# Kernel optimization log

Measured on AMD Instinct MI355X. Metric: run time of the kernel, lower is better.

## Reference

```python
import jax, jax.numpy as jnp
import numpy as np

EPS_NORM = 1e-12  # F.normalize eps
EPS_LOG = 1e-10
COMMITMENT_COST = 0.25


def setup_inputs() -> dict:
    key = jax.random.key(0)
    k1, k2 = jax.random.split(key)
    x = jax.random.normal(k1, (32, 256, 32, 32), dtype=jnp.float32)
    # nn.Embedding weight init: uniform(-1, 1)
    W = jax.random.uniform(k2, (1024, 256), dtype=jnp.float32, minval=-1.0, maxval=1.0)
    return {"x": x, "W": W, "n": 2}


def reference(x, W, n):
    sg = jax.lax.stop_gradient
    # NCHW -> NHWC
    inputs = jnp.transpose(x, (0, 2, 3, 1))
    B, H, Wd, D = inputs.shape
    K = W.shape[0]
    flat = inputs.reshape(-1, D)                       # [N, D]
    N = flat.shape[0]
    # squared euclidean distances via matmul: [N, K]
    distances = (jnp.sum(flat * flat, axis=1, keepdims=True)
                 + jnp.sum(W * W, axis=1)
                 - 2.0 * jnp.matmul(flat, W.T))
    # topk of -distances -> n smallest distances
    neg_vals, encoding_indices = jax.lax.top_k(-distances, n)  # [N, n]
    inv_dist = 1.0 / (-neg_vals)                        # 1/distance, [N, n]
    norm = jnp.maximum(jnp.sqrt(jnp.sum(inv_dist * inv_dist, axis=-1, keepdims=True)), EPS_NORM)
    weights = sg(inv_dist / norm)                       # detached in torch
    # scatter weights into one-hot-ish encodings [N, K]
    rows = jnp.arange(N)[:, None]
    encodings = jnp.zeros((N, K), dtype=flat.dtype).at[rows, encoding_indices].set(weights)
    quantized = jnp.matmul(encodings, W).reshape(B, H, Wd, D)
    e_latent_loss = jnp.mean((sg(quantized) - inputs) ** 2)
    q_latent_loss = jnp.mean((quantized - sg(inputs)) ** 2)
    loss = q_latent_loss + COMMITMENT_COST * e_latent_loss
    # straight-through
    quantized_st = inputs + sg(quantized - inputs)
    avg_probs = jnp.mean(encodings, axis=0)
    perplexity = jnp.exp(-jnp.sum(avg_probs * jnp.log(avg_probs + EPS_LOG)))
    return loss, jnp.transpose(quantized_st, (0, 3, 1, 2)), perplexity, encodings
```

## Files before the change

kernel.cpp:

```cpp
#include <hip/hip_runtime.h>
#include <math.h>

#define NROWS 32768
#define DIMS  256
#define KCODES 1024

typedef __attribute__((ext_vector_type(8))) short short8;
typedef __attribute__((ext_vector_type(4))) float f32x4;

static const size_t OFF_WB     = 8388608;
static const size_t OFF_WNORM  = OFF_WB + 131072;
static const size_t OFF_ENCSUM = OFF_WNORM + 1024;
static const size_t OFF_LOSSP  = OFF_ENCSUM + 1024;
static const size_t OFF_WND    = OFF_LOSSP + 8192;

static const size_t OUT_Q    = 1;
static const size_t OUT_PERP = 8388609;
static const size_t OUT_ENC  = 8388610;

__device__ inline unsigned short f2bf(float f) {
    unsigned int u = __float_as_uint(f);
    unsigned int r = u + 0x7FFFu + ((u >> 16) & 1u);
    return (unsigned short)(r >> 16);
}

__device__ inline float packdi(float d, int code) {
    return __uint_as_float((__float_as_uint(d) & 0xFFFFFC00u) | (unsigned)code);
}

__device__ __forceinline__ void gl_lds16(const void* gsrc, void* ldst) {
    typedef const __attribute__((address_space(1))) unsigned int GU;
    typedef __attribute__((address_space(3))) unsigned int LU;
    __builtin_amdgcn_global_load_lds((GU*)gsrc, (LU*)ldst, 16, 0, 0);
}

__global__ __launch_bounds__(256) void wprep(const float* __restrict__ Wm,
                                             unsigned short* __restrict__ Wb,
                                             float* __restrict__ wnorm,
                                             double* __restrict__ wnormd,
                                             float* __restrict__ enc_sum)
{
    const int r = blockIdx.x * 4 + (threadIdx.x >> 6);
    const int lane = threadIdx.x & 63;
    float4 v = ((const float4*)(Wm + (size_t)r * 256))[lane];
    ushort4 o;
    o.x = f2bf(v.x); o.y = f2bf(v.y); o.z = f2bf(v.z); o.w = f2bf(v.w);
    const int d0 = lane * 4;
    const int kk = d0 >> 5, quad = (d0 >> 3) & 3, jb = d0 & 7;
    const int tt = r >> 4, col = r & 15;
    const size_t idx = (size_t)tt * 4096 + (size_t)((kk * 4 + quad) * 16 + col) * 8 + jb;
    *(ushort4*)(Wb + idx) = o;
    double s = (double)v.x*(double)v.x + (double)v.y*(double)v.y
             + (double)v.z*(double)v.z + (double)v.w*(double)v.w;
    #pragma unroll
    for (int off = 32; off > 0; off >>= 1) s += __shfl_down(s, off);
    if (lane == 0) { wnormd[r] = s; wnorm[r] = (float)s; }
    if (blockIdx.x == 0) {
        #pragma unroll
        for (int q = 0; q < 4; ++q) enc_sum[threadIdx.x * 4 + q] = 0.0f;
    }
}

__global__ __launch_bounds__(256, 4) void gemm_topk_quant(
    const float* __restrict__ x, const unsigned short* __restrict__ Wb,
    const float* __restrict__ wnorm, const double* __restrict__ wnd,
    const float* __restrict__ Wm,
    float* __restrict__ enc_sum,
    float* __restrict__ enc,
    float* __restrict__ outq, float* __restrict__ loss_part)
{
    __shared__ __align__(16) char lds[36864];
    float*  sCd   = (float*)lds;
    int*    mIdx  = (int*)(lds + 13312);
    double* rd    = (double*)(lds + 14336);
    float*  qtile = (float*)lds;
    double* rnr   = (double*)(lds + 33792);
    int*    s0    = (int*)(lds + 34048);
    int*    s1    = (int*)(lds + 34176);
    float*  sw0   = (float*)(lds + 34304);
    float*  sw1   = (float*)(lds + 34432);
    double* sredd = (double*)(lds + 34560);
    unsigned short* xtile = (unsigned short*)(lds + 16384);
    float*  wnLds = (float*)(lds + 32768);

    const int t    = threadIdx.x;
    const int wave = t >> 6;
    const int g    = wave & 1;
    const int h    = wave >> 1;
    const int lane = t & 63;
    const int col  = lane & 15;
    const int quad = lane >> 4;
    const int r0   = blockIdx.x * 32;
    const int b    = r0 >> 10;
    const int hw0  = r0 & 1023;
    const float* xblk = x + (size_t)b * 262144 + hw0;

    const int row = t >> 3;
    const int q8  = t & 7;

    const char* wb_bytes = (const char*)Wb;
    {
        const char* src = wb_bytes + (size_t)(h * 32) * 8192 + g * 4096;
        char* dstl = lds + h * 8192 + g * 4096;
        #pragma unroll
        for (int q = 0; q < 4; ++q)
            gl_lds16(src + q * 1024 + lane * 16, dstl + q * 1024);
        gl_lds16((const char*)wnorm + wave * 1024 + lane * 16,
                 (char*)wnLds + wave * 1024);
    }

    float xs[32];
    {
        const float* xr = xblk + row;
        #pragma unroll
        for (int c = 0; c < 8; ++c)
            #pragma unroll
            for (int k = 0; k < 4; ++k)
                xs[c * 4 + k] = xr[(size_t)(c * 32 + q8 * 4 + k) * 1024];
    }

    #pragma unroll
    for (int c = 0; c < 8; ++c) {
        ushort4 o;
        o.x = f2bf(xs[c * 4 + 0]);
        o.y = f2bf(xs[c * 4 + 1]);
        o.z = f2bf(xs[c * 4 + 2]);
        o.w = f2bf(xs[c * 4 + 3]);
        const int xi = (row * 256 + c * 32 + q8 * 4) ^ ((row & 7) << 3);
        *(ushort4*)(xtile + xi) = o;
    }
    __syncthreads();

    short8 af[8];
    #pragma unroll
    for (int kk = 0; kk < 8; ++kk) {
        const int xi = ((g * 16 + col) * 256 + kk * 32 + quad * 8) ^ ((col & 7) << 3);
        af[kk] = *(const short8*)(xtile + xi);
    }
    __syncthreads();

    float m0[4], m1[4], m2[4];
    #pragma unroll
    for (int r = 0; r < 4; ++r) { m0[r] = 3.4e38f; m1[r] = 3.4e38f; m2[r] = 3.4e38f; }

    const f32x4 zero4 = {0.f, 0.f, 0.f, 0.f};
    for (int cc = 0; cc < 32; ++cc) {
        if (cc < 31) {
            const char* src = wb_bytes + (size_t)(h * 32 + cc + 1) * 8192 + g * 4096;
            char* dstl = lds + ((cc + 1) & 1) * 16384 + h * 8192 + g * 4096;
            #pragma unroll
            for (int q = 0; q < 4; ++q)
                gl_lds16(src + q * 1024 + lane * 16, dstl + q * 1024);
        }
        *(f32x4*)(enc + (size_t)(r0 + cc) * KCODES + t * 4) = zero4;

        const char* bb = lds + (cc & 1) * 16384 + h * 8192;
        f32x4 acc_a = {0.f, 0.f, 0.f, 0.f};
        f32x4 acc_b = {0.f, 0.f, 0.f, 0.f};
        #pragma unroll
        for (int kk = 0; kk < 4; ++kk) {
            short8 b0 = *(const short8*)(bb + kk * 1024 + lane * 16);
            short8 b1 = *(const short8*)(bb + (kk + 4) * 1024 + lane * 16);
            acc_a = __builtin_amdgcn_mfma_f32_16x16x32_bf16(af[kk], b0, acc_a, 0, 0, 0);
            acc_b = __builtin_amdgcn_mfma_f32_16x16x32_bf16(af[kk + 4], b1, acc_b, 0, 0, 0);
        }
        const int code0 = h * 512 + cc * 16 + col;
        const float wn0 = wnLds[code0];
        #pragma unroll
        for (int r = 0; r < 4; ++r) {
            float pv0 = packdi(fmaf(-2.0f, acc_a[r] + acc_b[r], wn0), code0);
            m2[r] = __builtin_amdgcn_fmed3f(m1[r], m2[r], pv0);
            m1[r] = __builtin_amdgcn_fmed3f(m0[r], m1[r], pv0);
            m0[r] = fminf(m0[r], pv0);
        }
        __syncthreads();
    }

    #pragma unroll
    for (int r = 0; r < 4; ++r) {
        const int rl = g * 16 + quad * 4 + r;
        const int s  = h * 48 + col * 3;
        sCd[(s + 0) * 34 + rl] = m0[r];
        sCd[(s + 1) * 34 + rl] = m1[r];
        sCd[(s + 2) * 34 + rl] = m2[r];
    }
    __syncthreads();

    {
        float a0 = 3.4e38f, a1 = 3.4e38f, a2 = 3.4e38f, a3 = 3.4e38f,
              a4 = 3.4e38f, a5 = 3.4e38f, a6 = 3.4e38f, a7 = 3.4e38f;
        #pragma unroll
        for (int i = 0; i < 12; ++i) {
            float d = sCd[(q8 * 12 + i) * 34 + row];
            if (d < a7) {
                a7 = d; float tf;
                if (a7 < a6) { tf = a7; a7 = a6; a6 = tf; }
                if (a6 < a5) { tf = a6; a6 = a5; a5 = tf; }
                if (a5 < a4) { tf = a5; a5 = a4; a4 = tf; }
                if (a4 < a3) { tf = a4; a4 = a3; a3 = tf; }
                if (a3 < a2) { tf = a3; a3 = a2; a2 = tf; }
                if (a2 < a1) { tf = a2; a2 = a1; a1 = tf; }
                if (a1 < a0) { tf = a1; a1 = a0; a0 = tf; }
            }
        }
        float sel = 3.4e38f;
        #pragma unroll
        for (int q = 0; q < 8; ++q) {
            float m = a0;
            m = fminf(m, __shfl_xor(m, 1));
            m = fminf(m, __shfl_xor(m, 2));
            m = fminf(m, __shfl_xor(m, 4));
            if (q8 == q) sel = m;
            if (a0 == m) { a0 = a1; a1 = a2; a2 = a3; a3 = a4;
                           a4 = a5; a5 = a6; a6 = a7; a7 = 3.4e38f; }
        }
        mIdx[row * 8 + q8] = (int)(__float_as_uint(sel) & 1023u);
    }
    __syncthreads();

    {
        int cd[8];
        #pragma unroll
        for (int c8 = 0; c8 < 8; ++c8) cd[c8] = mIdx[row * 8 + c8];
        double dot[8];
        #pragma unroll
        for (int c8 = 0; c8 < 8; ++c8) dot[c8] = 0.0;
        double rn = 0.0;
        #pragma unroll
        for (int c = 0; c < 8; ++c) {
            const int d0 = c * 32 + q8 * 4;
            const double x0 = (double)xs[c * 4 + 0];
            const double x1 = (double)xs[c * 4 + 1];
            const double x2 = (double)xs[c * 4 + 2];
            const double x3 = (double)xs[c * 4 + 3];
            rn += x0*x0 + x1*x1 + x2*x2 + x3*x3;
            #pragma unroll
            for (int c8 = 0; c8 < 8; ++c8) {
                const float4 wv = *(const float4*)(Wm + (size_t)cd[c8] * 256 + d0);
                dot[c8] += x0 * (double)wv.x + x1 * (double)wv.y
                         + x2 * (double)wv.z + x3 * (double)wv.w;
            }
        }
        #pragma unroll
        for (int m = 1; m < 8; m <<= 1) {
            #pragma unroll
            for (int c8 = 0; c8 < 8; ++c8) dot[c8] += __shfl_xor(dot[c8], m);
            rn += __shfl_xor(rn, m);
        }
        int myc = 0; double mydot = 0.0;
        #pragma unroll
        for (int c8 = 0; c8 < 8; ++c8)
            if (q8 == c8) { myc = cd[c8]; mydot = dot[c8]; }
        rd[row * 8 + q8] = wnd[myc] - 2.0 * mydot;
        if (q8 == 0) rnr[row] = rn;
    }
    __syncthreads();

    if (t < 32) {
        double rn = rnr[t];
        double d0 = 1e300, d1 = 1e300; int b0 = 1 << 30, b1 = 1 << 30;
        #pragma unroll
        for (int q = 0; q < 8; ++q) {
            double d = rd[t * 8 + q];
            int    c = mIdx[t * 8 + q];
            if (d < d0 || (d == d0 && c < b0)) { d1 = d0; b1 = b0; d0 = d; b0 = c; }
            else if (d < d1 || (d == d1 && c < b1)) { d1 = d; b1 = c; }
        }
        double D0 = rn + d0;
        double D1 = rn + d1;
        double inv0 = 1.0 / D0, inv1 = 1.0 / D1;
        double nrm = sqrt(inv0 * inv0 + inv1 * inv1);
        if (nrm < 1e-12) nrm = 1e-12;
        float w0 = (float)(inv0 / nrm);
        float w1 = (float)(inv1 / nrm);
        s0[t] = b0; s1[t] = b1; sw0[t] = w0; sw1[t] = w1;
        atomicAdd(&enc_sum[b0], w0);
        atomicAdd(&enc_sum[b1], w1);
        enc[(size_t)(r0 + t) * KCODES + b0] = w0;
        enc[(size_t)(r0 + t) * KCODES + b1] = w1;
    }
    __syncthreads();

    double ls = 0.0;
    #pragma unroll
    for (int p2 = 0; p2 < 2; ++p2) {
        const int   cA = s0[row], cB = s1[row];
        const float w0 = sw0[row], w1 = sw1[row];
        #pragma unroll
        for (int cq = 0; cq < 4; ++cq) {
            const int c  = p2 * 4 + cq;
            const int dg = c * 32 + q8 * 4;
            const float4 a  = *(const float4*)(Wm + (size_t)cA * 256 + dg);
            const float4 bv = *(const float4*)(Wm + (size_t)cB * 256 + dg);
            f32x4 qv;
            qv.x = w0 * a.x + w1 * bv.x;
            qv.y = w0 * a.y + w1 * bv.y;
            qv.z = w0 * a.z + w1 * bv.z;
            qv.w = w0 * a.w + w1 * bv.w;
            float e0 = qv.x - xs[c * 4 + 0];
            float e1 = qv.y - xs[c * 4 + 1];
            float e2 = qv.z - xs[c * 4 + 2];
            float e3 = qv.w - xs[c * 4 + 3];
            ls += (double)(e0*e0 + e1*e1 + e2*e2 + e3*e3);
            const int dl = cq * 32 + q8 * 4;
            *(f32x4*)(qtile + row * 132 + dl) = qv;
        }
        __syncthreads();
        #pragma unroll
        for (int p = 0; p < 4; ++p) {
            const int task = p * 256 + t;
            const int cl   = task >> 3;
            const int hwq  = task & 7;
            f32x4 v;
            v.x = qtile[(hwq * 4 + 0) * 132 + cl];
            v.y = qtile[(hwq * 4 + 1) * 132 + cl];
            v.z = qtile[(hwq * 4 + 2) * 132 + cl];
            v.w = qtile[(hwq * 4 + 3) * 132 + cl];
            *(f32x4*)(outq + ((size_t)(b * 256 + p2 * 128 + cl)) * 1024 + hw0 + hwq * 4) = v;
        }
        __syncthreads();
    }

    #pragma unroll
    for (int off = 32; off > 0; off >>= 1) ls += __shfl_down(ls, off);
    if (lane == 0) sredd[wave] = ls;
    __syncthreads();
    if (t == 0) {
        double s = 0.0;
        #pragma unroll
        for (int w = 0; w < 4; ++w) s += sredd[w];
        loss_part[blockIdx.x] = (float)s;
    }
}

__global__ __launch_bounds__(256) void finalize_k(const float* __restrict__ enc_sum,
                                                  const float* __restrict__ loss_part,
                                                  float* __restrict__ out)
{
    __shared__ double sh[256];
    const int t = threadIdx.x;
    double ls = 0.0;
    for (int i = t; i < 1024; i += 256) ls += (double)loss_part[i];
    sh[t] = ls; __syncthreads();
    for (int s = 128; s > 0; s >>= 1) { if (t < s) sh[t] += sh[t + s]; __syncthreads(); }
    double loss_sum = sh[0];
    __syncthreads();
    double ps = 0.0;
    for (int k = t; k < KCODES; k += 256) {
        double p = (double)enc_sum[k] / (double)NROWS;
        ps += p * log(p + 1e-10);
    }
    sh[t] = ps; __syncthreads();
    for (int s = 128; s > 0; s >>= 1) { if (t < s) sh[t] += sh[t + s]; __syncthreads(); }
    if (t == 0) {
        out[0]        = (float)(1.25 * loss_sum / 8388608.0);
        out[OUT_PERP] = (float)exp(-sh[0]);
    }
}

extern "C" void kernel_launch(void* const* d_in, const int* in_sizes, int n_in,
                              void* d_out, int out_size, void* d_ws, size_t ws_size,
                              hipStream_t stream)
{
    const float* x  = (const float*)d_in[0];
    const float* Wm = (const float*)d_in[1];
    float* out = (float*)d_out;
    float* ws  = (float*)d_ws;

    unsigned short* Wb      = (unsigned short*)(ws + OFF_WB);
    float*          wnorm   = ws + OFF_WNORM;
    float*          enc_sum = ws + OFF_ENCSUM;
    float*          loss_p  = ws + OFF_LOSSP;
    double*         wnd     = (double*)(ws + OFF_WND);

    wprep<<<KCODES / 4, 256, 0, stream>>>(Wm, Wb, wnorm, wnd, enc_sum);
    gemm_topk_quant<<<NROWS / 32, 256, 0, stream>>>(x, Wb, wnorm, wnd, Wm, enc_sum,
                                                    out + OUT_ENC, out + OUT_Q, loss_p);
    finalize_k<<<1, 256, 0, stream>>>(enc_sum, loss_p, out);
}
```

Before: 241.2 us.

## Coalesce x loads through an LDS transpose and merge quantized writeback passes

Input rows were read as strided scalar loads. They are now read as float4 vectors along the spatial axis and transposed through a swizzled fp32 LDS bounce buffer. Both the fp32 registers kept for the loss and the bf16 MFMA A-fragments are taken from that buffer, in two halves of the feature dimension. The quantized-output transpose also now uses one full 256-channel LDS tile instead of two half passes, which drops a pair of barriers. The cost is extra LDS traffic, added barriers during the load phase, and a larger LDS tile that has to fit the existing layout.

Result: no change. 238.1 us (-1.3%).

```diff
diff --git a/kernel.cpp b/kernel.cpp
--- a/kernel.cpp
+++ b/kernel.cpp
@@ -80,7 +80,7 @@
     float*  sw0   = (float*)(lds + 34304);
     float*  sw1   = (float*)(lds + 34432);
     double* sredd = (double*)(lds + 34560);
-    unsigned short* xtile = (unsigned short*)(lds + 16384);
+    float*  xbounce = (float*)(lds + 16384);
     float*  wnLds = (float*)(lds + 32768);
 
     const int t    = threadIdx.x;
@@ -110,32 +110,56 @@
     }
 
     float xs[32];
-    {
-        const float* xr = xblk + row;
-        #pragma unroll
-        for (int c = 0; c < 8; ++c)
+    short8 af[8];
+    const int hwq   = t & 7;
+    const int dbase = t >> 3;
+    const int arow  = g * 16 + col;
+    #pragma unroll
+    for (int h2 = 0; h2 < 2; ++h2) {
+        float4 xv0, xv1, xv2, xv3;
+        {
+            const float* xp = xblk + hwq * 4;
+            xv0 = *(const float4*)(xp + (size_t)(h2 * 128 +  0 + dbase) * 1024);
+            xv1 = *(const float4*)(xp + (size_t)(h2 * 128 + 32 + dbase) * 1024);
+            xv2 = *(const float4*)(xp + (size_t)(h2 * 128 + 64 + dbase) * 1024);
+            xv3 = *(const float4*)(xp + (size_t)(h2 * 128 + 96 + dbase) * 1024);
+        }
+        if (h2) __syncthreads();
+        #pragma unroll
+        for (int rr = 0; rr < 4; ++rr) {
+            const float4 xv = (rr == 0) ? xv0 : (rr == 1) ? xv1 : (rr == 2) ? xv2 : xv3;
+            const int dloc = rr * 32 + dbase;
             #pragma unroll
-            for (int k = 0; k < 4; ++k)
-                xs[c * 4 + k] = xr[(size_t)(c * 32 + q8 * 4 + k) * 1024];
-    }
-
-    #pragma unroll
-    for (int c = 0; c < 8; ++c) {
-        ushort4 o;
-        o.x = f2bf(xs[c * 4 + 0]);
-        o.y = f2bf(xs[c * 4 + 1]);
-        o.z = f2bf(xs[c * 4 + 2]);
-        o.w = f2bf(xs[c * 4 + 3]);
-        const int xi = (row * 256 + c * 32 + q8 * 4) ^ ((row & 7) << 3);
-        *(ushort4*)(xtile + xi) = o;
-    }
-    __syncthreads();
-
-    short8 af[8];
-    #pragma unroll
-    for (int kk = 0; kk < 8; ++kk) {
-        const int xi = ((g * 16 + col) * 256 + kk * 32 + quad * 8) ^ ((col & 7) << 3);
-        af[kk] = *(const short8*)(xtile + xi);
+            for (int j = 0; j < 4; ++j) {
+                const int hw = hwq * 4 + j;
+                const float vj = (j == 0) ? xv.x : (j == 1) ? xv.y : (j == 2) ? xv.z : xv.w;
+                xbounce[(hw * 128 + dloc) ^ ((hw & 7) << 2)] = vj;
+            }
+        }
+        __syncthreads();
+        #pragma unroll
+        for (int c2 = 0; c2 < 4; ++c2) {
+            const int w = (row * 128 + c2 * 32 + q8 * 4) ^ ((row & 7) << 2);
+            f32x4 v = *(const f32x4*)(xbounce + w);
+            xs[(h2 * 4 + c2) * 4 + 0] = v.x;
+            xs[(h2 * 4 + c2) * 4 + 1] = v.y;
+            xs[(h2 * 4 + c2) * 4 + 2] = v.z;
+            xs[(h2 * 4 + c2) * 4 + 3] = v.w;
+        }
+        #pragma unroll
+        for (int kk2 = 0; kk2 < 4; ++kk2) {
+            const int dloc = kk2 * 32 + quad * 8;
+            const int wA = (arow * 128 + dloc) ^ ((arow & 7) << 2);
+            const int wB = (arow * 128 + dloc + 4) ^ ((arow & 7) << 2);
+            f32x4 u = *(const f32x4*)(xbounce + wA);
+            f32x4 v = *(const f32x4*)(xbounce + wB);
+            short8 f;
+            f[0] = (short)f2bf(u.x); f[1] = (short)f2bf(u.y);
+            f[2] = (short)f2bf(u.z); f[3] = (short)f2bf(u.w);
+            f[4] = (short)f2bf(v.x); f[5] = (short)f2bf(v.y);
+            f[6] = (short)f2bf(v.z); f[7] = (short)f2bf(v.w);
+            af[h2 * 4 + kk2] = f;
+        }
     }
     __syncthreads();
 
@@ -282,13 +306,11 @@
     __syncthreads();
 
     double ls = 0.0;
-    #pragma unroll
-    for (int p2 = 0; p2 < 2; ++p2) {
+    {
         const int   cA = s0[row], cB = s1[row];
         const float w0 = sw0[row], w1 = sw1[row];
         #pragma unroll
-        for (int cq = 0; cq < 4; ++cq) {
-            const int c  = p2 * 4 + cq;
+        for (int c = 0; c < 8; ++c) {
             const int dg = c * 32 + q8 * 4;
             const float4 a  = *(const float4*)(Wm + (size_t)cA * 256 + dg);
             const float4 bv = *(const float4*)(Wm + (size_t)cB * 256 + dg);
@@ -302,23 +324,21 @@
             float e2 = qv.z - xs[c * 4 + 2];
             float e3 = qv.w - xs[c * 4 + 3];
             ls += (double)(e0*e0 + e1*e1 + e2*e2 + e3*e3);
-            const int dl = cq * 32 + q8 * 4;
-            *(f32x4*)(qtile + row * 132 + dl) = qv;
-        }
-        __syncthreads();
-        #pragma unroll
-        for (int p = 0; p < 4; ++p) {
-            const int task = p * 256 + t;
-            const int cl   = task >> 3;
-            const int hwq  = task & 7;
-            f32x4 v;
-            v.x = qtile[(hwq * 4 + 0) * 132 + cl];
-            v.y = qtile[(hwq * 4 + 1) * 132 + cl];
-            v.z = qtile[(hwq * 4 + 2) * 132 + cl];
-            v.w = qtile[(hwq * 4 + 3) * 132 + cl];
-            *(f32x4*)(outq + ((size_t)(b * 256 + p2 * 128 + cl)) * 1024 + hw0 + hwq * 4) = v;
-        }
-        __syncthreads();
+            *(f32x4*)(qtile + row * 264 + dg) = qv;
+        }
+    }
+    __syncthreads();
+    #pragma unroll
+    for (int p = 0; p < 8; ++p) {
+        const int task = p * 256 + t;
+        const int cl   = task >> 3;
+        const int hq   = task & 7;
+        f32x4 v;
+        v.x = qtile[(hq * 4 + 0) * 264 + cl];
+        v.y = qtile[(hq * 4 + 1) * 264 + cl];
+        v.z = qtile[(hq * 4 + 2) * 264 + cl];
+        v.w = qtile[(hq * 4 + 3) * 264 + cl];
+        *(f32x4*)(outq + ((size_t)(b * 256 + cl)) * 1024 + hw0 + hq * 4) = v;
     }
 
     #pragma unroll
```
